# Optimization experiments

Measured on AMD Instinct MI355X. Metric: run time of the kernel, lower is better.

The kernel has to match this reference:

```python
import jax, jax.numpy as jnp
import numpy as np

WS = 8        # window_size
HEADS = 8
HEAD_DIM = 32
DISP = WS // 2  # cyclic shift displacement (shifted=True)

# relative position indices, shape (WS^3, WS^3, 3), values in [0, 2*WS-2]
_coords = np.array([[x, y, z] for x in range(WS) for y in range(WS) for z in range(WS)])
REL_IDX = (_coords[None, :, :] - _coords[:, None, :]) + (WS - 1)


def setup_inputs() -> dict:
    key = jax.random.key(0)
    ks = jax.random.split(key, 5)
    dim = HEADS * HEAD_DIM  # 256
    x = jax.random.normal(ks[0], (2, 32, 32, 32, dim), dtype=jnp.float32)
    w_qkv = jax.random.normal(ks[1], (dim, 3 * dim), dtype=jnp.float32) * (dim ** -0.5)
    pos_embedding = jax.random.normal(ks[2], (2 * WS - 1, 2 * WS - 1, 2 * WS - 1), dtype=jnp.float32)
    w_out = jax.random.normal(ks[3], (dim, dim), dtype=jnp.float32) * (dim ** -0.5)
    b_out = jax.random.normal(ks[4], (dim,), dtype=jnp.float32) * 0.01
    return {"x": x, "w_qkv": w_qkv, "pos_embedding": pos_embedding, "w_out": w_out, "b_out": b_out}


def reference(x, w_qkv, pos_embedding, w_out, b_out):
    scale = HEAD_DIM ** -0.5
    # cyclic shift (shifted=True)
    x = jnp.roll(x, (-DISP, -DISP, -DISP), axis=(1, 2, 3))
    b, n_h, n_w, n_d, _ = x.shape
    nwh, nww, nwd = n_h // WS, n_w // WS, n_d // WS
    nw = nwh * nww * nwd
    t = WS ** 3  # tokens per window

    qkv = x @ w_qkv  # (b, n_h, n_w, n_d, 3*inner)
    qkv = qkv.reshape(b, nwh, WS, nww, WS, nwd, WS, 3, HEADS, HEAD_DIM)
    # -> (3, b, h, nwh, nww, nwd, wh, ww, wd, c)
    qkv = jnp.transpose(qkv, (7, 0, 8, 1, 3, 5, 2, 4, 6, 9))
    qkv = qkv.reshape(3, b, HEADS, nw, t, HEAD_DIM)
    q, k, v = qkv[0], qkv[1], qkv[2]

    dots = jnp.einsum('bhwid,bhwjd->bhwij', q, k) * scale
    bias = pos_embedding[REL_IDX[:, :, 0], REL_IDX[:, :, 1], REL_IDX[:, :, 2]]  # (t, t)
    dots = dots + bias
    attn = jax.nn.softmax(dots, axis=-1)
    out = jnp.einsum('bhwij,bhwjd->bhwid', attn, v)  # (b, h, nw, t, c)

    out = out.reshape(b, HEADS, nwh, nww, nwd, WS, WS, WS, HEAD_DIM)
    # -> (b, nwh, wh, nww, ww, nwd, wd, h, c)
    out = jnp.transpose(out, (0, 2, 5, 3, 6, 4, 7, 1, 8))
    out = out.reshape(b, n_h, n_w, n_d, HEADS * HEAD_DIM)
    out = out @ w_out + b_out
    # cyclic back shift
    out = jnp.roll(out, (DISP, DISP, DISP), axis=(1, 2, 3))
    return out
```

## Files before the change

### kernel.cpp

```cpp
#include <hip/hip_runtime.h>

typedef _Float16 h16;
typedef h16 h8_t __attribute__((ext_vector_type(8)));
typedef h16 h4_t __attribute__((ext_vector_type(4)));
typedef float f4_t __attribute__((ext_vector_type(4)));
typedef unsigned int u32;
typedef u32 u4_t __attribute__((ext_vector_type(4)));

#define LOG2E 1.4426950408889634f
#define QSCALE 0.25505998f
#define SOFF 4.0f

#define OFF_BIAS 0u
#define OFF_WQKV 524288u
#define OFF_WOUT 917504u
#define OFF_QKV  1048576u
#define WS_BBYTES 50331648u
#define WSTR_H    25165824u
#define KOFF_H    8388608u
#define VOFF_H    16777216u
#define VT_WH     16384u

static __device__ __forceinline__ u32 pkrtz(float a, float b) {
    return __builtin_bit_cast(u32, __builtin_amdgcn_cvt_pkrtz(a, b));
}
static __device__ __forceinline__ h4_t pk4(float a, float b, float c, float d) {
    uint2 t; t.x = pkrtz(a, b); t.y = pkrtz(c, d);
    return __builtin_bit_cast(h4_t, t);
}

__global__ __launch_bounds__(256) void k0_prep(const float* __restrict__ wqkv,
                                               const float* __restrict__ pos,
                                               const float* __restrict__ wout,
                                               h16* __restrict__ bias,
                                               h16* __restrict__ wT,
                                               h16* __restrict__ wToT)
{
    const int bid = blockIdx.x;
    const int e = bid * 256 + threadIdx.x;
    if (bid < 1024) {
        int o = e;
        int e4  = o & 3;
        int cf2 = (o >> 2) & 1;
        int c   = (o >> 3) & 15;
        int hi  = (o >> 7) & 3;
        int cfp = (o >> 9) & 1;
        int rf  = (o >> 10) & 1;
        int kc  = (o >> 11) & 15;
        int sq  = o >> 15;
        int i = sq * 64 + (cfp * 2 + cf2) * 16 + c;
        int j = kc * 32 + rf * 16 + hi * 4 + e4;
        int ix = i >> 6, iy = (i >> 3) & 7, iz = i & 7;
        int jx = j >> 6, jy = (j >> 3) & 7, jz = j & 7;
        int r0 = jx - ix + 7, r1 = jy - iy + 7, r2 = jz - iz + 7;
        float v = pos[(r0 * 15 + r1) * 15 + r2] * LOG2E - SOFF;
        bias[o] = (h16)v;
    } else if (bid < 1792) {
        int t = e - 1024 * 256;
        int n = t >> 8, k = t & 255;
        float v = wqkv[k * 768 + n];
        if (n < 256) v *= QSCALE;
        wT[n * 256 + k] = (h16)v;
    } else {
        int t = e - 1792 * 256;
        int n = t >> 8, k = t & 255;
        wToT[n * 256 + k] = (h16)wout[k * 256 + n];
    }
}

__global__ __launch_bounds__(768) __attribute__((amdgpu_waves_per_eu(3, 6)))
void k1_qkv(const float* __restrict__ x,
            const h16* __restrict__ wT,
            h16* __restrict__ qkv,
            unsigned long xstr, unsigned long wstr)
{
    __shared__ __align__(16) h16 xs[64 * 256];
    const int b = blockIdx.y;
    const float* xb = x + (unsigned long)b * xstr;
    h16* Qo = qkv + (unsigned long)b * wstr;
    h16* Ko = Qo + KOFF_H;
    h16* Vt = Qo + VOFF_H;

    const int tid = threadIdx.x;
    const int tile = blockIdx.x;
    const int st = tile & 7, w = tile >> 3;
    const int wh = w >> 4, ww = (w >> 2) & 3, wd = w & 3;
    const int Xs = (wh * 8 + st + 4) & 31;

    for (int i = tid; i < 4096; i += 768) {
        int row = i >> 6, seg = i & 63;
        int iw = row >> 3, id = row & 7;
        int Y = (ww * 8 + iw + 4) & 31, Z = (wd * 8 + id + 4) & 31;
        const float* xp = xb + ((Xs * 32 + Y) * 32 + Z) * 256 + seg * 4;
        f4_t v = *(const f4_t*)xp;
        uint2 tmp;
        tmp.x = pkrtz(v[0], v[1]);
        tmp.y = pkrtz(v[2], v[3]);
        *(uint2*)((char*)xs + row * 512 + (((u32)(seg * 8)) ^ ((u32)(row & 7) << 4))) = tmp;
    }
    __syncthreads();

    const int wv = tid >> 6, lane = tid & 63;
    const int c = lane & 15, hi = lane >> 4;
    f4_t acc[4][4];
#pragma unroll
    for (int i = 0; i < 4; ++i)
#pragma unroll
        for (int j = 0; j < 4; ++j) { f4_t z = {0.f, 0.f, 0.f, 0.f}; acc[i][j] = z; }

#pragma unroll 2
    for (int ks = 0; ks < 8; ++ks) {
        h8_t a[4], bfr[4];
#pragma unroll
        for (int rf = 0; rf < 4; ++rf)
            a[rf] = *(const h8_t*)(wT + (wv * 64 + rf * 16 + c) * 256 + ks * 32 + hi * 8);
#pragma unroll
        for (int cf = 0; cf < 4; ++cf) {
            int tok = cf * 16 + c;
            bfr[cf] = *(const h8_t*)((const char*)xs + tok * 512 +
                                     (((u32)(ks * 64 + hi * 16)) ^ ((u32)(tok & 7) << 4)));
        }
#pragma unroll
        for (int rf = 0; rf < 4; ++rf)
#pragma unroll
            for (int cf = 0; cf < 4; ++cf)
                acc[rf][cf] = __builtin_amdgcn_mfma_f32_16x16x32_f16(a[rf], bfr[cf], acc[rf][cf], 0, 0, 0);
    }

    const int wbh = w * 8;
    if (wv < 8) {
#pragma unroll
        for (int rf = 0; rf < 4; ++rf) {
            const int ch = wv * 64 + rf * 16 + hi * 4;
            const int sel = ch >> 8;
            const int ch2 = ch & 255, hh2 = ch2 >> 5, d0 = ch2 & 31;
#pragma unroll
            for (int cf = 0; cf < 4; ++cf) {
                const int t = st * 64 + cf * 16 + c;
                f4_t v = acc[rf][cf];
                h16* qp = (sel ? Ko : Qo) + ((wbh + hh2) * 512 + t) * 32 + d0;
                uint2 sv;
                sv.x = pkrtz(v[0], v[1]);
                sv.y = pkrtz(v[2], v[3]);
                *(uint2*)qp = sv;
            }
        }
    }
    __syncthreads();
    if (wv >= 8) {
#pragma unroll
        for (int rf = 0; rf < 4; ++rf) {
            const int ch2 = (wv - 8) * 64 + rf * 16 + hi * 4;
            const int hh2 = ch2 >> 5, d0 = ch2 & 31;
            const int bh = hh2 * 2048 + (d0 >> 4) * 512 + (d0 & 15) * 8;
#pragma unroll
            for (int cf = 0; cf < 4; ++cf) {
                const int tl = cf * 16 + c;
                const int bt = (tl >> 5) * 1024 + ((tl >> 2) & 3) * 128 +
                               ((tl >> 4) & 1) * 4 + (tl & 3);
                f4_t v = acc[rf][cf];
#pragma unroll
                for (int r = 0; r < 4; ++r)
                    xs[bh + bt + r * 8] = (h16)v[r];
            }
        }
    }
    __syncthreads();
    {
        h16* Vw = Vt + (unsigned long)wbh * VT_WH + st * 2048;
        for (int i = tid; i < 2048; i += 768) {
            const int hh2 = i >> 8, rem = i & 255;
            h8_t vchunk = *(const h8_t*)(xs + i * 8);
            *(h8_t*)(Vw + hh2 * VT_WH + rem * 8) = vchunk;
        }
    }
}

#define KA_PHASE(KFC, BBC, VVC, KFN, BBN, VVN, KC, PREF) do {                           \
    if (PREF) {                                                                         \
        const int kt1_ = ((KC) + 1) * 32;                                               \
        KFN[0] = *(const h8_t*)(Kp + (kt1_ + c) * 32 + hi * 8);                         \
        KFN[1] = *(const h8_t*)(Kp + (kt1_ + 16 + c) * 32 + hi * 8);                    \
        VVN[0] = *(const h8_t*)(Vp + ((KC) + 1) * 1024 + lane * 8);                     \
        VVN[1] = *(const h8_t*)(Vp + ((KC) + 1) * 1024 + 512 + lane * 8);               \
        _Pragma("unroll")                                                               \
        for (int t = 0; t < 4; ++t)                                                     \
            BBN[t] = *(const h8_t*)(Bq + (((KC) + 1) * 4 + t) * 512);                   \
    }                                                                                   \
    f4_t s[2][4];                                                                       \
    _Pragma("unroll")                                                                   \
    for (int rf = 0; rf < 2; ++rf)                                                      \
        _Pragma("unroll")                                                               \
        for (int cfp = 0; cfp < 2; ++cfp) {                                             \
            h8_t bv = BBC[rf * 2 + cfp];                                                \
            _Pragma("unroll")                                                           \
            for (int cf2 = 0; cf2 < 2; ++cf2) {                                         \
                const int cf = cfp * 2 + cf2;                                           \
                f4_t si;                                                                \
                si[0] = (float)bv[cf2 * 4 + 0];                                         \
                si[1] = (float)bv[cf2 * 4 + 1];                                         \
                si[2] = (float)bv[cf2 * 4 + 2];                                         \
                si[3] = (float)bv[cf2 * 4 + 3];                                         \
                s[rf][cf] = __builtin_amdgcn_mfma_f32_16x16x32_f16(KFC[rf], qf[cf], si, 0, 0, 0); \
            }                                                                           \
        }                                                                               \
    h4_t pa[2][4];                                                                      \
    _Pragma("unroll")                                                                   \
    for (int rf = 0; rf < 2; ++rf)                                                      \
        _Pragma("unroll")                                                               \
        for (int cf = 0; cf < 4; ++cf) {                                                \
            float p0 = __builtin_amdgcn_exp2f(s[rf][cf][0]);                            \
            float p1 = __builtin_amdgcn_exp2f(s[rf][cf][1]);                            \
            float p2 = __builtin_amdgcn_exp2f(s[rf][cf][2]);                            \
            float p3 = __builtin_amdgcn_exp2f(s[rf][cf][3]);                            \
            l[cf] += (p0 + p1) + (p2 + p3);                                             \
            pa[rf][cf] = pk4(p0, p1, p2, p3);                                           \
        }                                                                               \
    const u4_t vw0 = __builtin_bit_cast(u4_t, VVC[0]);                                  \
    const u4_t vw1 = __builtin_bit_cast(u4_t, VVC[1]);                                  \
    _Pragma("unroll")                                                                   \
    for (int rf = 0; rf < 2; ++rf) {                                                    \
        uint2 vt0; vt0.x = vw0[rf * 2]; vt0.y = vw0[rf * 2 + 1];                        \
        uint2 vt1; vt1.x = vw1[rf * 2]; vt1.y = vw1[rf * 2 + 1];                        \
        const h4_t vB0 = __builtin_bit_cast(h4_t, vt0);                                 \
        const h4_t vB1 = __builtin_bit_cast(h4_t, vt1);                                 \
        _Pragma("unroll")                                                               \
        for (int cf = 0; cf < 4; ++cf) {                                                \
            acc[cf][0] = __builtin_amdgcn_mfma_f32_16x16x16f16(pa[rf][cf], vB0, acc[cf][0], 0, 0, 0); \
            acc[cf][1] = __builtin_amdgcn_mfma_f32_16x16x16f16(pa[rf][cf], vB1, acc[cf][1], 0, 0, 0); \
        }                                                                               \
    }                                                                                   \
} while (0)

__global__ __launch_bounds__(512) __attribute__((amdgpu_waves_per_eu(2, 8)))
void ka_fused(const h16* __restrict__ qkv,
              const h16* __restrict__ Bi,
              const h16* __restrict__ wToT,
              const float* __restrict__ bout,
              float* __restrict__ out,
              unsigned long wstr, unsigned long ostr)
{
    __shared__ __align__(16) h16 as[64 * 264];
    const int b = blockIdx.y;
    const h16* qb = qkv + (unsigned long)b * wstr;
    float* outb = out + (unsigned long)b * ostr;

    const int tid = threadIdx.x;
    const int lane = tid & 63, hh = tid >> 6;
    const int c = lane & 15, hi = lane >> 4;
    const int bid = blockIdx.x;
    const int blk = (bid & 7) * 64 + (bid >> 3);
    const int sq = blk & 7, w = blk >> 3;
    const int qbase = sq * 64;
    const int base = w * 8 + hh;
    const h16* Qp = qb + base * (512 * 32);
    const h16* Kp = qb + KOFF_H + base * (512 * 32);
    const h16* Vp = qb + VOFF_H + base * VT_WH;
    const h16* Bq = Bi + sq * 32768 + (hi * 16 + c) * 8;

    h8_t qf[4];
#pragma unroll
    for (int cf = 0; cf < 4; ++cf)
        qf[cf] = *(const h8_t*)(Qp + (qbase + cf * 16 + c) * 32 + hi * 8);

    f4_t acc[4][2];
#pragma unroll
    for (int i = 0; i < 4; ++i)
#pragma unroll
        for (int j = 0; j < 2; ++j) { f4_t z = {0.f, 0.f, 0.f, 0.f}; acc[i][j] = z; }
    float l[4] = {0.f, 0.f, 0.f, 0.f};

    h8_t kfA[2], kfB[2];
    h8_t bbA[4], bbB[4];
    h8_t vvA[2], vvB[2];

    kfA[0] = *(const h8_t*)(Kp + c * 32 + hi * 8);
    kfA[1] = *(const h8_t*)(Kp + (16 + c) * 32 + hi * 8);
    vvA[0] = *(const h8_t*)(Vp + lane * 8);
    vvA[1] = *(const h8_t*)(Vp + 512 + lane * 8);
#pragma unroll
    for (int t = 0; t < 4; ++t)
        bbA[t] = *(const h8_t*)(Bq + t * 512);

#pragma unroll 1
    for (int kc2 = 0; kc2 < 8; ++kc2) {
        KA_PHASE(kfA, bbA, vvA, kfB, bbB, vvB, kc2 * 2, 1);
        KA_PHASE(kfB, bbB, vvB, kfA, bbA, vvA, kc2 * 2 + 1, kc2 < 7);
    }

#pragma unroll
    for (int cf = 0; cf < 4; ++cf) {
        l[cf] += __shfl_xor(l[cf], 16);
        l[cf] += __shfl_xor(l[cf], 32);
    }

#pragma unroll
    for (int cf = 0; cf < 4; ++cf) {
#pragma unroll
        for (int r = 0; r < 4; ++r) {
            float rl = __builtin_amdgcn_rcpf(__shfl(l[cf], hi * 4 + r));
            const int tok = cf * 16 + hi * 4 + r;
#pragma unroll
            for (int dh = 0; dh < 2; ++dh)
                as[tok * 264 + hh * 32 + dh * 16 + c] = (h16)(acc[cf][dh][r] * rl);
        }
    }
    __syncthreads();

    f4_t pacc[2][4];
#pragma unroll
    for (int i = 0; i < 2; ++i)
#pragma unroll
        for (int j = 0; j < 4; ++j) { f4_t z = {0.f, 0.f, 0.f, 0.f}; pacc[i][j] = z; }

#pragma unroll 2
    for (int ks = 0; ks < 8; ++ks) {
        h8_t a2[2], b2[4];
#pragma unroll
        for (int rf = 0; rf < 2; ++rf)
            a2[rf] = *(const h8_t*)(wToT + (hh * 32 + rf * 16 + c) * 256 + ks * 32 + hi * 8);
#pragma unroll
        for (int cf = 0; cf < 4; ++cf)
            b2[cf] = *(const h8_t*)(as + (cf * 16 + c) * 264 + ks * 32 + hi * 8);
#pragma unroll
        for (int rf = 0; rf < 2; ++rf)
#pragma unroll
            for (int cf = 0; cf < 4; ++cf)
                pacc[rf][cf] = __builtin_amdgcn_mfma_f32_16x16x32_f16(a2[rf], b2[cf], pacc[rf][cf], 0, 0, 0);
    }

    const int wh = w >> 4, ww = (w >> 2) & 3, wd = w & 3;
    const int X = (wh * 8 + sq + 4) & 31;
#pragma unroll
    for (int cf = 0; cf < 4; ++cf) {
        const int tl = cf * 16 + c;
        const int Y = (ww * 8 + (tl >> 3) + 4) & 31;
        const int Z = (wd * 8 + (tl & 7) + 4) & 31;
        float* op = outb + ((X * 32 + Y) * 32 + Z) * 256;
#pragma unroll
        for (int rf = 0; rf < 2; ++rf) {
            const int co = hh * 32 + rf * 16 + hi * 4;
            f4_t bo = *(const f4_t*)(bout + co);
            f4_t v = pacc[rf][cf];
            v[0] += bo[0]; v[1] += bo[1]; v[2] += bo[2]; v[3] += bo[3];
            *(f4_t*)(op + co) = v;
        }
    }
}

extern "C" void kernel_launch(void* const* d_in, const int* in_sizes, int n_in,
                              void* d_out, int out_size, void* d_ws, size_t ws_size,
                              hipStream_t stream)
{
    (void)in_sizes; (void)n_in; (void)out_size;
    const float* x    = (const float*)d_in[0];
    const float* wqkv = (const float*)d_in[1];
    const float* pos  = (const float*)d_in[2];
    const float* wout = (const float*)d_in[3];
    const float* bout = (const float*)d_in[4];
    float* out = (float*)d_out;
    char* ws = (char*)d_ws;

    h16* bias = (h16*)(ws + OFF_BIAS);
    h16* wT   = (h16*)(ws + OFF_WQKV);
    h16* wToT = (h16*)(ws + OFF_WOUT);
    h16* qkv  = (h16*)(ws + OFF_QKV);

    const unsigned long BSTR = 32768ul * 256ul;

    k0_prep<<<2048, 256, 0, stream>>>(wqkv, pos, wout, bias, wT, wToT);

    if (ws_size >= (size_t)OFF_QKV + 2ul * WS_BBYTES) {
        k1_qkv<<<dim3(512, 2), 768, 0, stream>>>(x, wT, qkv, BSTR, WSTR_H);
        ka_fused<<<dim3(512, 2), 512, 0, stream>>>(qkv, bias, wToT, bout, out, WSTR_H, BSTR);
    } else {
        for (int b = 0; b < 2; ++b) {
            k1_qkv<<<dim3(512, 1), 768, 0, stream>>>(x + b * BSTR, wT, qkv, 0, 0);
            ka_fused<<<dim3(512, 1), 512, 0, stream>>>(qkv, bias, wToT, bout, out + b * BSTR, 0, 0);
        }
    }
}
```

Baseline: 171.3 us.

## Split fused attention+projection into separate attention and projection kernels

Breaks the fused attention/output-projection kernel apart. The attention kernel now uses 256-thread blocks covering four heads each and writes a transposed fp16 attention output to a workspace buffer. A separate projection kernel loads that buffer into XOR-swizzled shared memory and runs the 256x256 projection with 64 output channels per wave. The goal is higher occupancy and better MFMA tiling in each stage, at the price of an extra round trip through global memory and two additional launches per batch.

Measured after the change: 185.5 us. +8.3%, slower.

```diff
diff --git a/kernel.cpp b/kernel.cpp
--- a/kernel.cpp
+++ b/kernel.cpp
@@ -20,6 +20,10 @@
 #define KOFF_H    8388608u
 #define VOFF_H    16777216u
 #define VT_WH     16384u
+#define OFF_AOT_P 101711872u
+#define NEED_P    118489088u
+#define OFF_AOT_F 51380224u
+#define NEED_F    68157440u
 
 static __device__ __forceinline__ u32 pkrtz(float a, float b) {
     return __builtin_bit_cast(u32, __builtin_amdgcn_cvt_pkrtz(a, b));
@@ -232,25 +236,18 @@
     }                                                                                   \
 } while (0)
 
-__global__ __launch_bounds__(512) __attribute__((amdgpu_waves_per_eu(2, 8)))
-void ka_fused(const h16* __restrict__ qkv,
-              const h16* __restrict__ Bi,
-              const h16* __restrict__ wToT,
-              const float* __restrict__ bout,
-              float* __restrict__ out,
-              unsigned long wstr, unsigned long ostr)
+__global__ __launch_bounds__(256) __attribute__((amdgpu_waves_per_eu(2, 8)))
+void k_attn(const h16* __restrict__ qb,
+            const h16* __restrict__ Bi,
+            h16* __restrict__ aot)
 {
-    __shared__ __align__(16) h16 as[64 * 264];
-    const int b = blockIdx.y;
-    const h16* qb = qkv + (unsigned long)b * wstr;
-    float* outb = out + (unsigned long)b * ostr;
-
     const int tid = threadIdx.x;
-    const int lane = tid & 63, hh = tid >> 6;
+    const int lane = tid & 63;
+    const int bid = blockIdx.x;
+    const int blk = (bid & 7) * 128 + (bid >> 3);
+    const int w = blk >> 4, sq = (blk >> 1) & 7, hgrp = blk & 1;
+    const int hh = hgrp * 4 + (tid >> 6);
     const int c = lane & 15, hi = lane >> 4;
-    const int bid = blockIdx.x;
-    const int blk = (bid & 7) * 64 + (bid >> 3);
-    const int sq = blk & 7, w = blk >> 3;
     const int qbase = sq * 64;
     const int base = w * 8 + hh;
     const h16* Qp = qb + base * (512 * 32);
@@ -294,43 +291,75 @@
         l[cf] += __shfl_xor(l[cf], 32);
     }
 
+    h16* Ap = aot + base * VT_WH;
 #pragma unroll
     for (int cf = 0; cf < 4; ++cf) {
-#pragma unroll
-        for (int r = 0; r < 4; ++r) {
-            float rl = __builtin_amdgcn_rcpf(__shfl(l[cf], hi * 4 + r));
-            const int tok = cf * 16 + hi * 4 + r;
-#pragma unroll
-            for (int dh = 0; dh < 2; ++dh)
-                as[tok * 264 + hh * 32 + dh * 16 + c] = (h16)(acc[cf][dh][r] * rl);
+        float rl0 = __builtin_amdgcn_rcpf(__shfl(l[cf], hi * 4 + 0));
+        float rl1 = __builtin_amdgcn_rcpf(__shfl(l[cf], hi * 4 + 1));
+        float rl2 = __builtin_amdgcn_rcpf(__shfl(l[cf], hi * 4 + 2));
+        float rl3 = __builtin_amdgcn_rcpf(__shfl(l[cf], hi * 4 + 3));
+#pragma unroll
+        for (int dh = 0; dh < 2; ++dh) {
+            uint2 sv;
+            sv.x = pkrtz(acc[cf][dh][0] * rl0, acc[cf][dh][1] * rl1);
+            sv.y = pkrtz(acc[cf][dh][2] * rl2, acc[cf][dh][3] * rl3);
+            *(uint2*)(Ap + (dh * 16 + c) * 512 + qbase + cf * 16 + hi * 4) = sv;
+        }
+    }
+}
+
+__global__ __launch_bounds__(256) __attribute__((amdgpu_waves_per_eu(3, 4)))
+void k_proj(const h16* __restrict__ aot,
+            const h16* __restrict__ wToT,
+            const float* __restrict__ bout,
+            float* __restrict__ outb)
+{
+    __shared__ __align__(16) h16 xs[64 * 256];
+    const int tid = threadIdx.x;
+    const int tile = blockIdx.x;
+    const int st = tile & 7, w = tile >> 3;
+
+    for (int i = tid; i < 2048; i += 256) {
+        const int ch = i >> 3, seg = i & 7;
+        h8_t v = *(const h8_t*)(aot + (unsigned long)(w * 8 + (ch >> 5)) * VT_WH +
+                                (ch & 31) * 512 + st * 64 + seg * 8);
+#pragma unroll
+        for (int t = 0; t < 8; ++t) {
+            const int tok = seg * 8 + t;
+            *(h16*)((char*)xs + tok * 512 + (((u32)(ch * 2)) ^ ((u32)t << 4))) = v[t];
         }
     }
     __syncthreads();
 
-    f4_t pacc[2][4];
-#pragma unroll
-    for (int i = 0; i < 2; ++i)
-#pragma unroll
-        for (int j = 0; j < 4; ++j) { f4_t z = {0.f, 0.f, 0.f, 0.f}; pacc[i][j] = z; }
+    const int wv = tid >> 6, lane = tid & 63;
+    const int c = lane & 15, hi = lane >> 4;
+    f4_t acc[4][4];
+#pragma unroll
+    for (int i = 0; i < 4; ++i)
+#pragma unroll
+        for (int j = 0; j < 4; ++j) { f4_t z = {0.f, 0.f, 0.f, 0.f}; acc[i][j] = z; }
 
 #pragma unroll 2
     for (int ks = 0; ks < 8; ++ks) {
-        h8_t a2[2], b2[4];
-#pragma unroll
-        for (int rf = 0; rf < 2; ++rf)
-            a2[rf] = *(const h8_t*)(wToT + (hh * 32 + rf * 16 + c) * 256 + ks * 32 + hi * 8);
-#pragma unroll
-        for (int cf = 0; cf < 4; ++cf)
-            b2[cf] = *(const h8_t*)(as + (cf * 16 + c) * 264 + ks * 32 + hi * 8);
-#pragma unroll
-        for (int rf = 0; rf < 2; ++rf)
+        h8_t a[4], bfr[4];
+#pragma unroll
+        for (int rf = 0; rf < 4; ++rf)
+            a[rf] = *(const h8_t*)(wToT + (wv * 64 + rf * 16 + c) * 256 + ks * 32 + hi * 8);
+#pragma unroll
+        for (int cf = 0; cf < 4; ++cf) {
+            int tok = cf * 16 + c;
+            bfr[cf] = *(const h8_t*)((const char*)xs + tok * 512 +
+                                     (((u32)(ks * 64 + hi * 16)) ^ ((u32)(tok & 7) << 4)));
+        }
+#pragma unroll
+        for (int rf = 0; rf < 4; ++rf)
 #pragma unroll
             for (int cf = 0; cf < 4; ++cf)
-                pacc[rf][cf] = __builtin_amdgcn_mfma_f32_16x16x32_f16(a2[rf], b2[cf], pacc[rf][cf], 0, 0, 0);
+                acc[rf][cf] = __builtin_amdgcn_mfma_f32_16x16x32_f16(a[rf], bfr[cf], acc[rf][cf], 0, 0, 0);
     }
 
     const int wh = w >> 4, ww = (w >> 2) & 3, wd = w & 3;
-    const int X = (wh * 8 + sq + 4) & 31;
+    const int X = (wh * 8 + st + 4) & 31;
 #pragma unroll
     for (int cf = 0; cf < 4; ++cf) {
         const int tl = cf * 16 + c;
@@ -338,10 +367,10 @@
         const int Z = (wd * 8 + (tl & 7) + 4) & 31;
         float* op = outb + ((X * 32 + Y) * 32 + Z) * 256;
 #pragma unroll
-        for (int rf = 0; rf < 2; ++rf) {
-            const int co = hh * 32 + rf * 16 + hi * 4;
+        for (int rf = 0; rf < 4; ++rf) {
+            const int co = wv * 64 + rf * 16 + hi * 4;
             f4_t bo = *(const f4_t*)(bout + co);
-            f4_t v = pacc[rf][cf];
+            f4_t v = acc[rf][cf];
             v[0] += bo[0]; v[1] += bo[1]; v[2] += bo[2]; v[3] += bo[3];
             *(f4_t*)(op + co) = v;
         }
@@ -370,13 +399,19 @@
 
     k0_prep<<<2048, 256, 0, stream>>>(wqkv, pos, wout, bias, wT, wToT);
 
-    if (ws_size >= (size_t)OFF_QKV + 2ul * WS_BBYTES) {
+    if (ws_size >= (size_t)NEED_P) {
+        h16* aot = (h16*)(ws + OFF_AOT_P);
         k1_qkv<<<dim3(512, 2), 768, 0, stream>>>(x, wT, qkv, BSTR, WSTR_H);
-        ka_fused<<<dim3(512, 2), 512, 0, stream>>>(qkv, bias, wToT, bout, out, WSTR_H, BSTR);
+        for (int b = 0; b < 2; ++b) {
+            k_attn<<<1024, 256, 0, stream>>>(qkv + (unsigned long)b * WSTR_H, bias, aot);
+            k_proj<<<512, 256, 0, stream>>>(aot, wToT, bout, out + (unsigned long)b * BSTR);
+        }
     } else {
+        h16* aot = (h16*)(ws + OFF_AOT_F);
         for (int b = 0; b < 2; ++b) {
-            k1_qkv<<<dim3(512, 1), 768, 0, stream>>>(x + b * BSTR, wT, qkv, 0, 0);
-            ka_fused<<<dim3(512, 1), 512, 0, stream>>>(qkv, bias, wToT, bout, out + b * BSTR, 0, 0);
-        }
-    }
-}
+            k1_qkv<<<dim3(512, 1), 768, 0, stream>>>(x + (unsigned long)b * BSTR, wT, qkv, 0, 0);
+            k_attn<<<1024, 256, 0, stream>>>(qkv, bias, aot);
+            k_proj<<<512, 256, 0, stream>>>(aot, wToT, bout, out + (unsigned long)b * BSTR);
+        }
+    }
+}
```
